# Performance work log

Measured on AMD Instinct MI355X. Metric: run time of the kernel, lower is better.

The kernel has to match this reference:

```python
import jax, jax.numpy as jnp
import numpy as np

# Hyperparameters matching init_kwargs
LR = 0.02
AT = 0.3
DSBETA = 0.1
EPS_DS = 0.5

B, D, N = 8192, 1024, 4096


def setup_inputs() -> dict:
    key = jax.random.key(0)
    k0, k1, k2, k3 = jax.random.split(key, 4)
    x = jax.random.normal(k0, (B, D), dtype=jnp.float32)
    weights = jax.random.normal(k1, (N, D), dtype=jnp.float32)
    relevance = jax.random.uniform(k2, (N, D), dtype=jnp.float32)
    moving_avg = jax.random.uniform(k3, (N, D), dtype=jnp.float32)
    node_control = jnp.ones((N,), dtype=jnp.float32)
    return {"x": x, "weights": weights, "relevance": relevance,
            "moving_avg": moving_avg, "node_control": node_control}


def reference(x, weights, relevance, moving_avg, node_control):
    n, d = weights.shape
    # pairwise squared distances [B, N] via one GEMM
    x2 = jnp.sum(x * x, axis=1, keepdims=True)            # [B,1]
    w2 = jnp.sum(weights * weights, axis=1)[None, :]      # [1,N]
    dists = x2 + w2 - 2.0 * jnp.matmul(x, weights.T)      # [B,N]
    # weighted_distance + activation
    rsum = jnp.sum(relevance, axis=1)                     # [N]
    dw = dists * (rsum / d)[None, :]
    dw = jnp.where(jnp.isnan(dw), 0.0, dw)
    act = (rsum[None, :] / (rsum[None, :] + dw + 1e-7)) * node_control[None, :]
    act_max = jnp.max(act, axis=1)                        # [B]
    idx = jnp.argmax(act, axis=1)                         # [B] winner per sample
    # high-activation mask; group samples by winner node (unique_node_diff_vectorized
    # == per-node mean of assigned high samples, done with segment_sum at fixed N)
    high = (act_max >= AT).astype(x.dtype)                # [B]
    counts = jax.ops.segment_sum(high, idx, num_segments=n)               # [N]
    sums = jax.ops.segment_sum(x * high[:, None], idx, num_segments=n)    # [N,D]
    has = (counts > 0).astype(x.dtype)[:, None]           # [N,1] nodes with >=1 high sample
    mean_s = sums / jnp.maximum(counts, 1.0)[:, None]     # [N,D] updatable_samples (dense)
    # update_node math (EMA moving_avg -> relevance -> weight update)
    a = LR * DSBETA
    distance = jnp.abs(mean_s - weights)
    mavg_new = a * distance + (1.0 - a) * moving_avg
    mx = jnp.max(mavg_new, axis=1, keepdims=True)
    mn = jnp.min(mavg_new, axis=1, keepdims=True)
    avg = jnp.mean(mavg_new, axis=1, keepdims=True)
    rel_new = 1.0 / (1.0 + jnp.exp((mavg_new - avg) / (EPS_DS * (mx - mn))))
    rel_new = jnp.where(jnp.isnan(rel_new), 1.0, rel_new)
    w_new = weights + LR * (mean_s - weights)
    # Original returns rows only for unique winning nodes (dynamic shape); here we
    # return fixed-shape [N,D] arrays masked to zero for nodes with no high sample.
    return (mean_s * has, w_new * has, rel_new * has)
```

## Files before the change

### kernel.cpp

```cpp
#include <hip/hip_runtime.h>
#include <stdint.h>

#define B_DIM 8192
#define D_DIM 1024
#define N_DIM 4096
#define ND ((size_t)N_DIM * D_DIM)
#define LRc 0.02f
#define ATc 0.3f
#define EMAc (0.02f * 0.1f)
#define QS 32.0f
#define INV_QS2 (1.0f / (QS * QS))
#define MARGIN_G 10.0f

typedef int intv4 __attribute__((ext_vector_type(4)));

__device__ __forceinline__ void async16(void* lds, const void* g) {
    __builtin_amdgcn_global_load_lds((const __attribute__((address_space(1))) void*)g,
                                     (__attribute__((address_space(3))) void*)lds, 16, 0, 0);
}

__device__ __forceinline__ int q8(float v) {
    return (int)rintf(fminf(fmaxf(v * QS, -127.0f), 127.0f));
}

__global__ __launch_bounds__(256) void prep(const float* __restrict__ x, const float* __restrict__ w,
                                            const float* __restrict__ rel,
                                            signed char* __restrict__ xq, signed char* __restrict__ wq,
                                            float* __restrict__ x2, float* __restrict__ w2,
                                            float* __restrict__ rsum, float* __restrict__ gb) {
    const int t = threadIdx.x;
    __shared__ float r1[4], r2s[4];
    if (blockIdx.x < B_DIM) {
        const int b = blockIdx.x;
        const float4 v = ((const float4*)(x + (size_t)b * D_DIM))[t];
        float ss = v.x * v.x + v.y * v.y + v.z * v.z + v.w * v.w;
        unsigned pk = (unsigned)(q8(v.x) & 255) | ((unsigned)(q8(v.y) & 255) << 8)
                    | ((unsigned)(q8(v.z) & 255) << 16) | ((unsigned)(q8(v.w) & 255) << 24);
        ((unsigned*)(xq + (size_t)b * D_DIM))[t] = pk;
#pragma unroll
        for (int o = 32; o; o >>= 1) ss += __shfl_xor(ss, o);
        if ((t & 63) == 0) r1[t >> 6] = ss;
        __syncthreads();
        if (t == 0) x2[b] = r1[0] + r1[1] + r1[2] + r1[3];
    } else {
        const int n = blockIdx.x - B_DIM;
        const float4 v = ((const float4*)(w + (size_t)n * D_DIM))[t];
        const float4 rv = ((const float4*)(rel + (size_t)n * D_DIM))[t];
        float ss = v.x * v.x + v.y * v.y + v.z * v.z + v.w * v.w;
        float rs = rv.x + rv.y + rv.z + rv.w;
        unsigned pk = (unsigned)(q8(v.x) & 255) | ((unsigned)(q8(v.y) & 255) << 8)
                    | ((unsigned)(q8(v.z) & 255) << 16) | ((unsigned)(q8(v.w) & 255) << 24);
        ((unsigned*)(wq + (size_t)n * D_DIM))[t] = pk;
#pragma unroll
        for (int o = 32; o; o >>= 1) { ss += __shfl_xor(ss, o); rs += __shfl_xor(rs, o); }
        if ((t & 63) == 0) { r1[t >> 6] = ss; r2s[t >> 6] = rs; }
        __syncthreads();
        if (t == 0) {
            const float w2v = r1[0] + r1[1] + r1[2] + r1[3];
            const float rsv = r2s[0] + r2s[1] + r2s[2] + r2s[3];
            w2[n] = w2v;
            rsum[n] = rsv;
            gb[n] = w2v + (1e-7f * (float)D_DIM) / rsv;
        }
    }
}

__global__ __launch_bounds__(256, 2) void gemm_g(const signed char* __restrict__ xq,
                                                 const signed char* __restrict__ wq,
                                                 const float* __restrict__ gb,
                                                 unsigned char* __restrict__ res,
                                                 float* __restrict__ tminp) {
    __shared__ int4 As[1024];
    __shared__ int4 Bs[2048];
    const int t = threadIdx.x;
    const int mt = blockIdx.x & 63;
    const int nt = blockIdx.x >> 6;
    const int m0 = mt * 128, n0 = nt * 256;
    const int lane = t & 63, wave = t >> 6;
    const int q = lane >> 4, ln = lane & 15;
    const int wm = wave >> 1, wn = wave & 1;

    intv4 acc[4][8];
#pragma unroll
    for (int i = 0; i < 4; ++i)
#pragma unroll
        for (int j = 0; j < 8; ++j) acc[i][j] = (intv4){0, 0, 0, 0};

    int rrA[4], jjA[4], rrB[8], jjB[8];
#pragma unroll
    for (int it = 0; it < 4; ++it) {
        int L = t + it * 256;
        rrA[it] = L >> 3; jjA[it] = (L & 7) ^ (rrA[it] & 7);
    }
#pragma unroll
    for (int it = 0; it < 8; ++it) {
        int L = t + it * 256;
        rrB[it] = L >> 3; jjB[it] = (L & 7) ^ (rrB[it] & 7);
    }

    const signed char* Ap = xq + (size_t)m0 * D_DIM;
    const signed char* Bp = wq + (size_t)n0 * D_DIM;
    for (int kt = 0; kt < 8; ++kt) {
        const int k0 = kt * 128;
#pragma unroll
        for (int it = 0; it < 4; ++it)
            async16((char*)As + (t + it * 256) * 16, Ap + (size_t)rrA[it] * D_DIM + k0 + jjA[it] * 16);
#pragma unroll
        for (int it = 0; it < 8; ++it)
            async16((char*)Bs + (t + it * 256) * 16, Bp + (size_t)rrB[it] * D_DIM + k0 + jjB[it] * 16);
        __syncthreads();
#pragma unroll
        for (int ks = 0; ks < 2; ++ks) {
            intv4 a[4], b[8];
#pragma unroll
            for (int i = 0; i < 4; ++i) {
                int r = wm * 64 + i * 16 + ln;
                int jx = (ks * 4 + q) ^ (r & 7);
                a[i] = *(const intv4*)((const char*)As + (r * 8 + jx) * 16);
            }
#pragma unroll
            for (int j = 0; j < 8; ++j) {
                int r = wn * 128 + j * 16 + ln;
                int jx = (ks * 4 + q) ^ (r & 7);
                b[j] = *(const intv4*)((const char*)Bs + (r * 8 + jx) * 16);
            }
#pragma unroll
            for (int i = 0; i < 4; ++i)
#pragma unroll
                for (int j = 0; j < 8; ++j)
                    acc[i][j] = __builtin_amdgcn_mfma_i32_16x16x64_i8(a[i], b[j], acc[i][j], 0, 0, 0);
        }
        __syncthreads();
    }

    float gbv[8];
#pragma unroll
    for (int j = 0; j < 8; ++j) gbv[j] = gb[n0 + wn * 128 + j * 16 + ln];
    const float cf = 2.0f * INV_QS2;
#pragma unroll
    for (int i = 0; i < 4; ++i) {
#pragma unroll
        for (int r = 0; r < 4; ++r) {
            const int m = m0 + wm * 64 + i * 16 + q * 4 + r;
            float g[8];
            float mnA = 3.4e38f, mnB = 3.4e38f;
#pragma unroll
            for (int j = 0; j < 8; ++j) {
                g[j] = gbv[j] - cf * (float)acc[i][j][r];
                if (j < 4) mnA = fminf(mnA, g[j]); else mnB = fminf(mnB, g[j]);
            }
#pragma unroll
            for (int o = 1; o < 16; o <<= 1) {
                mnA = fminf(mnA, __shfl_xor(mnA, o));
                mnB = fminf(mnB, __shfl_xor(mnB, o));
            }
            if (ln == 0) {
                tminp[(size_t)m * 64 + nt * 4 + wn * 2 + 0] = mnA;
                tminp[(size_t)m * 64 + nt * 4 + wn * 2 + 1] = mnB;
            }
#pragma unroll
            for (int j = 0; j < 8; ++j) {
                const float base = (j < 4) ? mnA : mnB;
                int u = (int)rintf((g[j] - base) * 2.0f);
                u = (u > 255) ? 255 : u;
                res[(size_t)m * N_DIM + n0 + wn * 128 + j * 16 + ln] = (unsigned char)u;
            }
        }
    }
}

__global__ __launch_bounds__(256) void resolve(const unsigned char* __restrict__ res,
                                               const float* __restrict__ tminp,
                                               const float* __restrict__ x2p,
                                               const float* __restrict__ x, const float* __restrict__ w,
                                               const float* __restrict__ w2, const float* __restrict__ rsum,
                                               const float* __restrict__ ncp,
                                               int* __restrict__ win) {
    const int lane = threadIdx.x & 63, wave = threadIdx.x >> 6;
    const int b = blockIdx.x * 4 + wave;
    const float tv = tminp[(size_t)b * 64 + lane];
    float rowmin = tv;
#pragma unroll
    for (int o = 32; o; o >>= 1) rowmin = fminf(rowmin, __shfl_xor(rowmin, o));
    const float th = rowmin + MARGIN_G;
    const unsigned long long tmask = __ballot(tv <= th);
    const float x2v = x2p[b];

    int cnt = 0, myn = -1;
    float myg = 0.0f;
    unsigned long long tm = tmask;
    while (tm) {
        const int tt = __ffsll((long long)tm) - 1;
        tm &= tm - 1;
        const float tb = __shfl(tv, tt);
        const unsigned char rv = res[(size_t)b * N_DIM + tt * 64 + lane];
        const float g = tb + 0.5f * (float)rv;
        const bool c = (g <= th);
        cnt += __popcll(__ballot(c));
        if (c && myn < 0) { myn = tt * 64 + lane; myg = g; }
    }

    if (cnt == 1) {
        if (myn >= 0) {
            const float act = ncp[myn] * (float)D_DIM / ((float)D_DIM + x2v + myg);
            win[b] = (act >= ATc) ? myn : -1;
        }
    } else {
        const float4* xr = (const float4*)(x + (size_t)b * D_DIM);
        float4 xv[4];
#pragma unroll
        for (int j = 0; j < 4; ++j) xv[j] = xr[lane + j * 64];
        float best_act = -1.0f;
        int best_n = N_DIM;
        tm = tmask;
        while (tm) {
            const int tt = __ffsll((long long)tm) - 1;
            tm &= tm - 1;
            const float tb = __shfl(tv, tt);
            const unsigned char rv = res[(size_t)b * N_DIM + tt * 64 + lane];
            const float g = tb + 0.5f * (float)rv;
            unsigned long long cm = __ballot(g <= th);
            while (cm) {
                const int l = __ffsll((long long)cm) - 1;
                cm &= cm - 1;
                const int n = tt * 64 + l;
                const float4* wr = (const float4*)(w + (size_t)n * D_DIM);
                float p = 0.f;
#pragma unroll
                for (int j = 0; j < 4; ++j) {
                    const float4 wv = wr[lane + j * 64];
                    p += xv[j].x * wv.x + xv[j].y * wv.y + xv[j].z * wv.z + xv[j].w * wv.w;
                }
#pragma unroll
                for (int o = 32; o; o >>= 1) p += __shfl_xor(p, o);
                const float dist = x2v + w2[n] - 2.0f * p;
                const float rs = rsum[n];
                const float dw = dist * rs * (1.0f / (float)D_DIM);
                const float a = rs * ncp[n] / (rs + dw + 1e-7f);
                if (a > best_act || (a == best_act && n < best_n)) { best_act = a; best_n = n; }
            }
        }
        if (lane == 0) win[b] = (best_act >= ATc) ? best_n : -1;
    }
}

__global__ __launch_bounds__(256) void finalize(const float* __restrict__ x, const float* __restrict__ w,
                                                const float* __restrict__ mavg, const int* __restrict__ win,
                                                float* __restrict__ out) {
    const int n = blockIdx.x, t = threadIdx.x;
    __shared__ unsigned short list[B_DIM];
    __shared__ int cnt;
    if (t == 0) cnt = 0;
    __syncthreads();
    const int4* wp = (const int4*)win;
#pragma unroll
    for (int k = 0; k < 8; ++k) {
        const int4 v = wp[k * 256 + t];
        const int b0 = (k * 256 + t) * 4;
        if (v.x == n) list[atomicAdd(&cnt, 1)] = (unsigned short)(b0 + 0);
        if (v.y == n) list[atomicAdd(&cnt, 1)] = (unsigned short)(b0 + 1);
        if (v.z == n) list[atomicAdd(&cnt, 1)] = (unsigned short)(b0 + 2);
        if (v.w == n) list[atomicAdd(&cnt, 1)] = (unsigned short)(b0 + 3);
    }
    __syncthreads();
    const int c = cnt;
    float4 s = {0.f, 0.f, 0.f, 0.f};
    for (int e = 0; e < c; ++e) {
        const float4 xv = ((const float4*)(x + (size_t)list[e] * D_DIM))[t];
        s.x += xv.x; s.y += xv.y; s.z += xv.z; s.w += xv.w;
    }
    const float has = (c > 0) ? 1.0f : 0.0f;
    const float invc = 1.0f / fmaxf((float)c, 1.0f);
    const size_t base4 = (size_t)n * (D_DIM / 4);
    const float4 wv = ((const float4*)w)[base4 + t];
    const float4 mk = ((const float4*)mavg)[base4 + t];
    float4 ms, mv;
    ms.x = s.x * invc; ms.y = s.y * invc; ms.z = s.z * invc; ms.w = s.w * invc;
    mv.x = EMAc * fabsf(ms.x - wv.x) + (1.0f - EMAc) * mk.x;
    mv.y = EMAc * fabsf(ms.y - wv.y) + (1.0f - EMAc) * mk.y;
    mv.z = EMAc * fabsf(ms.z - wv.z) + (1.0f - EMAc) * mk.z;
    mv.w = EMAc * fabsf(ms.w - wv.w) + (1.0f - EMAc) * mk.w;
    float lmax = fmaxf(fmaxf(mv.x, mv.y), fmaxf(mv.z, mv.w));
    float lmin = fminf(fminf(mv.x, mv.y), fminf(mv.z, mv.w));
    float lsum = mv.x + mv.y + mv.z + mv.w;
#pragma unroll
    for (int o = 32; o; o >>= 1) {
        lmax = fmaxf(lmax, __shfl_xor(lmax, o));
        lmin = fminf(lmin, __shfl_xor(lmin, o));
        lsum += __shfl_xor(lsum, o);
    }
    __shared__ float smax[4], smin[4], ssum[4];
    const int wave = t >> 6, lane = t & 63;
    if (lane == 0) { smax[wave] = lmax; smin[wave] = lmin; ssum[wave] = lsum; }
    __syncthreads();
    const float mx = fmaxf(fmaxf(smax[0], smax[1]), fmaxf(smax[2], smax[3]));
    const float mn = fminf(fminf(smin[0], smin[1]), fminf(smin[2], smin[3]));
    const float avg = (ssum[0] + ssum[1] + ssum[2] + ssum[3]) * (1.0f / (float)D_DIM);
    const float scale = 0.5f * (mx - mn);
    const float invs = (scale > 0.0f) ? 1.0f / scale : 0.0f;
    float4 relv;
    if (scale > 0.0f) {
        relv.x = 1.0f / (1.0f + __expf((mv.x - avg) * invs));
        relv.y = 1.0f / (1.0f + __expf((mv.y - avg) * invs));
        relv.z = 1.0f / (1.0f + __expf((mv.z - avg) * invs));
        relv.w = 1.0f / (1.0f + __expf((mv.w - avg) * invs));
    } else {
        relv.x = relv.y = relv.z = relv.w = 1.0f;
    }
    float4* o0 = (float4*)out;
    float4 r0, r1, r2;
    r0.x = ms.x * has; r0.y = ms.y * has; r0.z = ms.z * has; r0.w = ms.w * has;
    r1.x = (wv.x + LRc * (ms.x - wv.x)) * has;
    r1.y = (wv.y + LRc * (ms.y - wv.y)) * has;
    r1.z = (wv.z + LRc * (ms.z - wv.z)) * has;
    r1.w = (wv.w + LRc * (ms.w - wv.w)) * has;
    r2.x = relv.x * has; r2.y = relv.y * has; r2.z = relv.z * has; r2.w = relv.w * has;
    o0[base4 + t] = r0;
    o0[ND / 4 + base4 + t] = r1;
    o0[2 * (ND / 4) + base4 + t] = r2;
}

extern "C" void kernel_launch(void* const* d_in, const int* in_sizes, int n_in,
                              void* d_out, int out_size, void* d_ws, size_t ws_size,
                              hipStream_t stream) {
    const float* x    = (const float*)d_in[0];
    const float* w    = (const float*)d_in[1];
    const float* rel  = (const float*)d_in[2];
    const float* mavg = (const float*)d_in[3];
    const float* nc   = (const float*)d_in[4];
    float* out = (float*)d_out;

    char* p = (char*)d_ws;
    size_t off = 0;
    auto take = [&](size_t bytes) -> char* {
        char* r = p + off;
        off += (bytes + 255) & ~(size_t)255;
        return r;
    };
    signed char* xq = (signed char*)take((size_t)B_DIM * D_DIM);
    signed char* wq = (signed char*)take((size_t)N_DIM * D_DIM);
    float* x2       = (float*)take((size_t)B_DIM * 4);
    float* w2       = (float*)take((size_t)N_DIM * 4);
    float* rsum     = (float*)take((size_t)N_DIM * 4);
    float* gb       = (float*)take((size_t)N_DIM * 4);
    unsigned char* res = (unsigned char*)take((size_t)B_DIM * N_DIM);
    float* tminp    = (float*)take((size_t)B_DIM * 64 * 4);
    int* win        = (int*)take((size_t)B_DIM * 4);

    prep<<<B_DIM + N_DIM, 256, 0, stream>>>(x, w, rel, xq, wq, x2, w2, rsum, gb);
    gemm_g<<<1024, 256, 0, stream>>>(xq, wq, gb, res, tminp);
    resolve<<<B_DIM / 4, 256, 0, stream>>>(res, tminp, x2, x, w, w2, rsum, nc, win);
    finalize<<<N_DIM, 256, 0, stream>>>(x, w, mavg, win, out);
}
```

Before: 205.6 us.

## Fuse pipeline into persistent cooperative kernel with grid syncs and smaller GEMM tiles

```diff
diff --git a/kernel.cpp b/kernel.cpp
--- a/kernel.cpp
+++ b/kernel.cpp
@@ -1,5 +1,8 @@
 #include <hip/hip_runtime.h>
+#include <hip/hip_cooperative_groups.h>
 #include <stdint.h>
+
+namespace cg = cooperative_groups;
 
 #define B_DIM 8192
 #define D_DIM 1024
@@ -11,6 +14,7 @@
 #define QS 32.0f
 #define INV_QS2 (1.0f / (QS * QS))
 #define MARGIN_G 10.0f
+#define NBLK 512
 
 typedef int intv4 __attribute__((ext_vector_type(4)));
 
@@ -23,79 +27,73 @@
     return (int)rintf(fminf(fmaxf(v * QS, -127.0f), 127.0f));
 }
 
-__global__ __launch_bounds__(256) void prep(const float* __restrict__ x, const float* __restrict__ w,
-                                            const float* __restrict__ rel,
-                                            signed char* __restrict__ xq, signed char* __restrict__ wq,
-                                            float* __restrict__ x2, float* __restrict__ w2,
-                                            float* __restrict__ rsum, float* __restrict__ gb) {
-    const int t = threadIdx.x;
-    __shared__ float r1[4], r2s[4];
-    if (blockIdx.x < B_DIM) {
-        const int b = blockIdx.x;
-        const float4 v = ((const float4*)(x + (size_t)b * D_DIM))[t];
-        float ss = v.x * v.x + v.y * v.y + v.z * v.z + v.w * v.w;
-        unsigned pk = (unsigned)(q8(v.x) & 255) | ((unsigned)(q8(v.y) & 255) << 8)
-                    | ((unsigned)(q8(v.z) & 255) << 16) | ((unsigned)(q8(v.w) & 255) << 24);
-        ((unsigned*)(xq + (size_t)b * D_DIM))[t] = pk;
+__device__ __forceinline__ unsigned pack4(float4 v) {
+    return (unsigned)(q8(v.x) & 255) | ((unsigned)(q8(v.y) & 255) << 8)
+         | ((unsigned)(q8(v.z) & 255) << 16) | ((unsigned)(q8(v.w) & 255) << 24);
+}
+
+
+__device__ __forceinline__ void prep_row(int row, const float* x, const float* w, const float* rel,
+                                         signed char* xq, signed char* wq,
+                                         float* x2p, float* w2p, float* rsump, float* gbp, int lane) {
+    if (row < B_DIM) {
+        const float4* xr = (const float4*)(x + (size_t)row * D_DIM);
+        unsigned* xqr = (unsigned*)(xq + (size_t)row * D_DIM);
+        float ss = 0.f;
+#pragma unroll
+        for (int j = 0; j < 4; ++j) {
+            const float4 v = xr[lane + j * 64];
+            ss += v.x * v.x + v.y * v.y + v.z * v.z + v.w * v.w;
+            xqr[lane + j * 64] = pack4(v);
+        }
 #pragma unroll
         for (int o = 32; o; o >>= 1) ss += __shfl_xor(ss, o);
-        if ((t & 63) == 0) r1[t >> 6] = ss;
-        __syncthreads();
-        if (t == 0) x2[b] = r1[0] + r1[1] + r1[2] + r1[3];
+        if (lane == 0) x2p[row] = ss;
     } else {
-        const int n = blockIdx.x - B_DIM;
-        const float4 v = ((const float4*)(w + (size_t)n * D_DIM))[t];
-        const float4 rv = ((const float4*)(rel + (size_t)n * D_DIM))[t];
-        float ss = v.x * v.x + v.y * v.y + v.z * v.z + v.w * v.w;
-        float rs = rv.x + rv.y + rv.z + rv.w;
-        unsigned pk = (unsigned)(q8(v.x) & 255) | ((unsigned)(q8(v.y) & 255) << 8)
-                    | ((unsigned)(q8(v.z) & 255) << 16) | ((unsigned)(q8(v.w) & 255) << 24);
-        ((unsigned*)(wq + (size_t)n * D_DIM))[t] = pk;
+        const int n = row - B_DIM;
+        const float4* wr = (const float4*)(w + (size_t)n * D_DIM);
+        const float4* rr = (const float4*)(rel + (size_t)n * D_DIM);
+        unsigned* wqr = (unsigned*)(wq + (size_t)n * D_DIM);
+        float ss = 0.f, rs = 0.f;
+#pragma unroll
+        for (int j = 0; j < 4; ++j) {
+            const float4 v = wr[lane + j * 64];
+            const float4 rv = rr[lane + j * 64];
+            ss += v.x * v.x + v.y * v.y + v.z * v.z + v.w * v.w;
+            rs += rv.x + rv.y + rv.z + rv.w;
+            wqr[lane + j * 64] = pack4(v);
+        }
 #pragma unroll
         for (int o = 32; o; o >>= 1) { ss += __shfl_xor(ss, o); rs += __shfl_xor(rs, o); }
-        if ((t & 63) == 0) { r1[t >> 6] = ss; r2s[t >> 6] = rs; }
-        __syncthreads();
-        if (t == 0) {
-            const float w2v = r1[0] + r1[1] + r1[2] + r1[3];
-            const float rsv = r2s[0] + r2s[1] + r2s[2] + r2s[3];
-            w2[n] = w2v;
-            rsum[n] = rsv;
-            gb[n] = w2v + (1e-7f * (float)D_DIM) / rsv;
-        }
-    }
-}
-
-__global__ __launch_bounds__(256, 2) void gemm_g(const signed char* __restrict__ xq,
-                                                 const signed char* __restrict__ wq,
-                                                 const float* __restrict__ gb,
-                                                 unsigned char* __restrict__ res,
-                                                 float* __restrict__ tminp) {
-    __shared__ int4 As[1024];
-    __shared__ int4 Bs[2048];
-    const int t = threadIdx.x;
-    const int mt = blockIdx.x & 63;
-    const int nt = blockIdx.x >> 6;
-    const int m0 = mt * 128, n0 = nt * 256;
+        if (lane == 0) {
+            w2p[n] = ss;
+            rsump[n] = rs;
+            gbp[n] = ss + (1e-7f * (float)D_DIM) / rs;
+        }
+    }
+}
+
+__device__ __forceinline__ void gemm_tile(int tile, const signed char* xq, const signed char* wq,
+                                          const float* gbp, unsigned char* res, float* tminp,
+                                          int4* As, int4* Bs, int t) {
     const int lane = t & 63, wave = t >> 6;
     const int q = lane >> 4, ln = lane & 15;
     const int wm = wave >> 1, wn = wave & 1;
-
-    intv4 acc[4][8];
+    const int mt = tile & 63;
+    const int nt = tile >> 6;
+    const int m0 = mt * 128, n0 = nt * 128;
+
+    intv4 acc[4][4];
 #pragma unroll
     for (int i = 0; i < 4; ++i)
 #pragma unroll
-        for (int j = 0; j < 8; ++j) acc[i][j] = (intv4){0, 0, 0, 0};
-
-    int rrA[4], jjA[4], rrB[8], jjB[8];
-#pragma unroll
-    for (int it = 0; it < 4; ++it) {
-        int L = t + it * 256;
-        rrA[it] = L >> 3; jjA[it] = (L & 7) ^ (rrA[it] & 7);
-    }
-#pragma unroll
-    for (int it = 0; it < 8; ++it) {
-        int L = t + it * 256;
-        rrB[it] = L >> 3; jjB[it] = (L & 7) ^ (rrB[it] & 7);
+        for (int j = 0; j < 4; ++j) acc[i][j] = (intv4){0, 0, 0, 0};
+
+    int rr[4], jj[4];
+#pragma unroll
+    for (int s = 0; s < 4; ++s) {
+        int L = t + s * 256;
+        rr[s] = L >> 3; jj[s] = (L & 7) ^ (rr[s] & 7);
     }
 
     const signed char* Ap = xq + (size_t)m0 * D_DIM;
@@ -103,15 +101,14 @@
     for (int kt = 0; kt < 8; ++kt) {
         const int k0 = kt * 128;
 #pragma unroll
-        for (int it = 0; it < 4; ++it)
-            async16((char*)As + (t + it * 256) * 16, Ap + (size_t)rrA[it] * D_DIM + k0 + jjA[it] * 16);
-#pragma unroll
-        for (int it = 0; it < 8; ++it)
-            async16((char*)Bs + (t + it * 256) * 16, Bp + (size_t)rrB[it] * D_DIM + k0 + jjB[it] * 16);
+        for (int s = 0; s < 4; ++s) {
+            async16((char*)As + (t + s * 256) * 16, Ap + (size_t)rr[s] * D_DIM + k0 + jj[s] * 16);
+            async16((char*)Bs + (t + s * 256) * 16, Bp + (size_t)rr[s] * D_DIM + k0 + jj[s] * 16);
+        }
         __syncthreads();
 #pragma unroll
         for (int ks = 0; ks < 2; ++ks) {
-            intv4 a[4], b[8];
+            intv4 a[4], b[4];
 #pragma unroll
             for (int i = 0; i < 4; ++i) {
                 int r = wm * 64 + i * 16 + ln;
@@ -119,65 +116,53 @@
                 a[i] = *(const intv4*)((const char*)As + (r * 8 + jx) * 16);
             }
 #pragma unroll
-            for (int j = 0; j < 8; ++j) {
-                int r = wn * 128 + j * 16 + ln;
+            for (int j = 0; j < 4; ++j) {
+                int r = wn * 64 + j * 16 + ln;
                 int jx = (ks * 4 + q) ^ (r & 7);
                 b[j] = *(const intv4*)((const char*)Bs + (r * 8 + jx) * 16);
             }
 #pragma unroll
             for (int i = 0; i < 4; ++i)
 #pragma unroll
-                for (int j = 0; j < 8; ++j)
+                for (int j = 0; j < 4; ++j)
                     acc[i][j] = __builtin_amdgcn_mfma_i32_16x16x64_i8(a[i], b[j], acc[i][j], 0, 0, 0);
         }
         __syncthreads();
     }
 
-    float gbv[8];
-#pragma unroll
-    for (int j = 0; j < 8; ++j) gbv[j] = gb[n0 + wn * 128 + j * 16 + ln];
+    float gbv[4];
+#pragma unroll
+    for (int jt = 0; jt < 4; ++jt) gbv[jt] = gbp[n0 + wn * 64 + jt * 16 + ln];
     const float cf = 2.0f * INV_QS2;
 #pragma unroll
     for (int i = 0; i < 4; ++i) {
 #pragma unroll
         for (int r = 0; r < 4; ++r) {
             const int m = m0 + wm * 64 + i * 16 + q * 4 + r;
-            float g[8];
-            float mnA = 3.4e38f, mnB = 3.4e38f;
-#pragma unroll
-            for (int j = 0; j < 8; ++j) {
-                g[j] = gbv[j] - cf * (float)acc[i][j][r];
-                if (j < 4) mnA = fminf(mnA, g[j]); else mnB = fminf(mnB, g[j]);
+            float g[4];
+            float gmin = 3.4e38f;
+#pragma unroll
+            for (int jt = 0; jt < 4; ++jt) {
+                g[jt] = gbv[jt] - cf * (float)acc[i][jt][r];
+                gmin = fminf(gmin, g[jt]);
             }
 #pragma unroll
-            for (int o = 1; o < 16; o <<= 1) {
-                mnA = fminf(mnA, __shfl_xor(mnA, o));
-                mnB = fminf(mnB, __shfl_xor(mnB, o));
+            for (int o = 1; o < 16; o <<= 1) gmin = fminf(gmin, __shfl_xor(gmin, o));
+            if (ln == 0) tminp[(size_t)m * 64 + nt * 2 + wn] = gmin;
+#pragma unroll
+            for (int jt = 0; jt < 4; ++jt) {
+                int u = (int)rintf((g[jt] - gmin) * 2.0f);
+                u = (u > 255) ? 255 : u;
+                res[(size_t)m * N_DIM + n0 + wn * 64 + jt * 16 + ln] = (unsigned char)u;
             }
-            if (ln == 0) {
-                tminp[(size_t)m * 64 + nt * 4 + wn * 2 + 0] = mnA;
-                tminp[(size_t)m * 64 + nt * 4 + wn * 2 + 1] = mnB;
-            }
-#pragma unroll
-            for (int j = 0; j < 8; ++j) {
-                const float base = (j < 4) ? mnA : mnB;
-                int u = (int)rintf((g[j] - base) * 2.0f);
-                u = (u > 255) ? 255 : u;
-                res[(size_t)m * N_DIM + n0 + wn * 128 + j * 16 + ln] = (unsigned char)u;
-            }
-        }
-    }
-}
-
-__global__ __launch_bounds__(256) void resolve(const unsigned char* __restrict__ res,
-                                               const float* __restrict__ tminp,
-                                               const float* __restrict__ x2p,
-                                               const float* __restrict__ x, const float* __restrict__ w,
-                                               const float* __restrict__ w2, const float* __restrict__ rsum,
-                                               const float* __restrict__ ncp,
-                                               int* __restrict__ win) {
-    const int lane = threadIdx.x & 63, wave = threadIdx.x >> 6;
-    const int b = blockIdx.x * 4 + wave;
+        }
+    }
+}
+
+__device__ __forceinline__ void resolve_row(int b, const unsigned char* res, const float* tminp,
+                                            const float* x2p, const float* x, const float* w,
+                                            const float* w2p, const float* rsump, const float* ncp,
+                                            int* win, int lane) {
     const float tv = tminp[(size_t)b * 64 + lane];
     float rowmin = tv;
 #pragma unroll
@@ -233,8 +218,8 @@
                 }
 #pragma unroll
                 for (int o = 32; o; o >>= 1) p += __shfl_xor(p, o);
-                const float dist = x2v + w2[n] - 2.0f * p;
-                const float rs = rsum[n];
+                const float dist = x2v + w2p[n] - 2.0f * p;
+                const float rs = rsump[n];
                 const float dw = dist * rs * (1.0f / (float)D_DIM);
                 const float a = rs * ncp[n] / (rs + dw + 1e-7f);
                 if (a > best_act || (a == best_act && n < best_n)) { best_act = a; best_n = n; }
@@ -244,29 +229,32 @@
     }
 }
 
-__global__ __launch_bounds__(256) void finalize(const float* __restrict__ x, const float* __restrict__ w,
-                                                const float* __restrict__ mavg, const int* __restrict__ win,
-                                                float* __restrict__ out) {
-    const int n = blockIdx.x, t = threadIdx.x;
-    __shared__ unsigned short list[B_DIM];
-    __shared__ int cnt;
-    if (t == 0) cnt = 0;
+struct FinalSmem {
+    unsigned short list[B_DIM];
+    int cnt;
+    float smax[4], smin[4], ssum[4];
+};
+
+__device__ __forceinline__ void finalize_node(int n, const float* x, const float* w, const float* mavg,
+                                              const int* win, float* out, FinalSmem* sf, int t) {
+    const int lane = t & 63, wave = t >> 6;
+    if (t == 0) sf->cnt = 0;
     __syncthreads();
     const int4* wp = (const int4*)win;
 #pragma unroll
     for (int k = 0; k < 8; ++k) {
         const int4 v = wp[k * 256 + t];
         const int b0 = (k * 256 + t) * 4;
-        if (v.x == n) list[atomicAdd(&cnt, 1)] = (unsigned short)(b0 + 0);
-        if (v.y == n) list[atomicAdd(&cnt, 1)] = (unsigned short)(b0 + 1);
-        if (v.z == n) list[atomicAdd(&cnt, 1)] = (unsigned short)(b0 + 2);
-        if (v.w == n) list[atomicAdd(&cnt, 1)] = (unsigned short)(b0 + 3);
+        if (v.x == n) sf->list[atomicAdd(&sf->cnt, 1)] = (unsigned short)(b0 + 0);
+        if (v.y == n) sf->list[atomicAdd(&sf->cnt, 1)] = (unsigned short)(b0 + 1);
+        if (v.z == n) sf->list[atomicAdd(&sf->cnt, 1)] = (unsigned short)(b0 + 2);
+        if (v.w == n) sf->list[atomicAdd(&sf->cnt, 1)] = (unsigned short)(b0 + 3);
     }
     __syncthreads();
-    const int c = cnt;
+    const int c = sf->cnt;
     float4 s = {0.f, 0.f, 0.f, 0.f};
     for (int e = 0; e < c; ++e) {
-        const float4 xv = ((const float4*)(x + (size_t)list[e] * D_DIM))[t];
+        const float4 xv = ((const float4*)(x + (size_t)sf->list[e] * D_DIM))[t];
         s.x += xv.x; s.y += xv.y; s.z += xv.z; s.w += xv.w;
     }
     const float has = (c > 0) ? 1.0f : 0.0f;
@@ -289,13 +277,11 @@
         lmin = fminf(lmin, __shfl_xor(lmin, o));
         lsum += __shfl_xor(lsum, o);
     }
-    __shared__ float smax[4], smin[4], ssum[4];
-    const int wave = t >> 6, lane = t & 63;
-    if (lane == 0) { smax[wave] = lmax; smin[wave] = lmin; ssum[wave] = lsum; }
+    if (lane == 0) { sf->smax[wave] = lmax; sf->smin[wave] = lmin; sf->ssum[wave] = lsum; }
     __syncthreads();
-    const float mx = fmaxf(fmaxf(smax[0], smax[1]), fmaxf(smax[2], smax[3]));
-    const float mn = fminf(fminf(smin[0], smin[1]), fminf(smin[2], smin[3]));
-    const float avg = (ssum[0] + ssum[1] + ssum[2] + ssum[3]) * (1.0f / (float)D_DIM);
+    const float mx = fmaxf(fmaxf(sf->smax[0], sf->smax[1]), fmaxf(sf->smax[2], sf->smax[3]));
+    const float mn = fminf(fminf(sf->smin[0], sf->smin[1]), fminf(sf->smin[2], sf->smin[3]));
+    const float avg = (sf->ssum[0] + sf->ssum[1] + sf->ssum[2] + sf->ssum[3]) * (1.0f / (float)D_DIM);
     const float scale = 0.5f * (mx - mn);
     const float invs = (scale > 0.0f) ? 1.0f / scale : 0.0f;
     float4 relv;
@@ -318,6 +304,85 @@
     o0[base4 + t] = r0;
     o0[ND / 4 + base4 + t] = r1;
     o0[2 * (ND / 4) + base4 + t] = r2;
+}
+
+
+union SMem {
+    struct { int4 As[1024]; int4 Bs[1024]; } g;
+    FinalSmem f;
+};
+
+__global__ __launch_bounds__(256, 2) void som_fused(
+        const float* __restrict__ x, const float* __restrict__ w,
+        const float* __restrict__ rel, const float* __restrict__ mavg,
+        const float* __restrict__ ncp, float* __restrict__ out,
+        signed char* __restrict__ xq, signed char* __restrict__ wq,
+        float* __restrict__ x2p, float* __restrict__ w2p,
+        float* __restrict__ rsump, float* __restrict__ gbp,
+        unsigned char* __restrict__ res, float* __restrict__ tminp,
+        int* __restrict__ win) {
+    cg::grid_group grid = cg::this_grid();
+    __shared__ SMem sm;
+    const int t = threadIdx.x;
+    const int lane = t & 63, wave = t >> 6;
+
+    for (int it = 0; it < 6; ++it)
+        prep_row(((blockIdx.x + it * NBLK) << 2) + wave, x, w, rel, xq, wq, x2p, w2p, rsump, gbp, lane);
+
+    __threadfence(); grid.sync(); __threadfence();
+
+    for (int it = 0; it < 4; ++it)
+        gemm_tile(blockIdx.x + it * NBLK, xq, wq, gbp, res, tminp, sm.g.As, sm.g.Bs, t);
+
+    __threadfence(); grid.sync(); __threadfence();
+
+    for (int it = 0; it < 4; ++it)
+        resolve_row(((blockIdx.x + it * NBLK) << 2) + wave, res, tminp, x2p, x, w, w2p, rsump, ncp, win, lane);
+
+    __threadfence(); grid.sync(); __threadfence();
+
+    for (int it = 0; it < 8; ++it) {
+        __syncthreads();
+        finalize_node(blockIdx.x + it * NBLK, x, w, mavg, win, out, &sm.f, t);
+    }
+}
+
+
+__global__ __launch_bounds__(256) void prep_k(const float* __restrict__ x, const float* __restrict__ w,
+                                              const float* __restrict__ rel,
+                                              signed char* __restrict__ xq, signed char* __restrict__ wq,
+                                              float* __restrict__ x2p, float* __restrict__ w2p,
+                                              float* __restrict__ rsump, float* __restrict__ gbp) {
+    const int lane = threadIdx.x & 63, wave = threadIdx.x >> 6;
+    prep_row((blockIdx.x << 2) + wave, x, w, rel, xq, wq, x2p, w2p, rsump, gbp, lane);
+}
+
+__global__ __launch_bounds__(256) void gemm_k(const signed char* __restrict__ xq,
+                                              const signed char* __restrict__ wq,
+                                              const float* __restrict__ gbp,
+                                              unsigned char* __restrict__ res,
+                                              float* __restrict__ tminp) {
+    __shared__ int4 As[1024];
+    __shared__ int4 Bs[1024];
+    gemm_tile(blockIdx.x, xq, wq, gbp, res, tminp, As, Bs, threadIdx.x);
+}
+
+__global__ __launch_bounds__(256) void resolve_k(const unsigned char* __restrict__ res,
+                                                 const float* __restrict__ tminp,
+                                                 const float* __restrict__ x2p,
+                                                 const float* __restrict__ x, const float* __restrict__ w,
+                                                 const float* __restrict__ w2p, const float* __restrict__ rsump,
+                                                 const float* __restrict__ ncp,
+                                                 int* __restrict__ win) {
+    const int lane = threadIdx.x & 63, wave = threadIdx.x >> 6;
+    resolve_row((blockIdx.x << 2) + wave, res, tminp, x2p, x, w, w2p, rsump, ncp, win, lane);
+}
+
+__global__ __launch_bounds__(256) void finalize_k(const float* __restrict__ x, const float* __restrict__ w,
+                                                  const float* __restrict__ mavg, const int* __restrict__ win,
+                                                  float* __restrict__ out) {
+    __shared__ FinalSmem sf;
+    finalize_node(blockIdx.x, x, w, mavg, win, out, &sf, threadIdx.x);
 }
 
 extern "C" void kernel_launch(void* const* d_in, const int* in_sizes, int n_in,
@@ -347,8 +412,15 @@
     float* tminp    = (float*)take((size_t)B_DIM * 64 * 4);
     int* win        = (int*)take((size_t)B_DIM * 4);
 
-    prep<<<B_DIM + N_DIM, 256, 0, stream>>>(x, w, rel, xq, wq, x2, w2, rsum, gb);
-    gemm_g<<<1024, 256, 0, stream>>>(xq, wq, gb, res, tminp);
-    resolve<<<B_DIM / 4, 256, 0, stream>>>(res, tminp, x2, x, w, w2, rsum, nc, win);
-    finalize<<<N_DIM, 256, 0, stream>>>(x, w, mavg, win, out);
-}
+    void* kargs[] = { (void*)&x, (void*)&w, (void*)&rel, (void*)&mavg, (void*)&nc, (void*)&out,
+                      (void*)&xq, (void*)&wq, (void*)&x2, (void*)&w2, (void*)&rsum, (void*)&gb,
+                      (void*)&res, (void*)&tminp, (void*)&win };
+    hipError_t err = hipLaunchCooperativeKernel((const void*)som_fused, dim3(NBLK), dim3(256),
+                                                kargs, 0, stream);
+    if (err != hipSuccess) {
+        prep_k<<<(B_DIM + N_DIM) / 4, 256, 0, stream>>>(x, w, rel, xq, wq, x2, w2, rsum, gb);
+        gemm_k<<<2048, 256, 0, stream>>>(xq, wq, gb, res, tminp);
+        resolve_k<<<B_DIM / 4, 256, 0, stream>>>(res, tminp, x2, x, w, w2, rsum, nc, win);
+        finalize_k<<<N_DIM, 256, 0, stream>>>(x, w, mavg, win, out);
+    }
+}
```

After: 661.7 us. 3.22x slower.

## Pack GEMM candidate scores into 4-bit nibbles and use one wave per row in prep

Applied to the files above, without the earlier changes.

```diff
diff --git a/kernel.cpp b/kernel.cpp
--- a/kernel.cpp
+++ b/kernel.cpp
@@ -1,5 +1,6 @@
 #include <hip/hip_runtime.h>
 #include <stdint.h>
+
 
 #define B_DIM 8192
 #define D_DIM 1024
@@ -23,52 +24,59 @@
     return (int)rintf(fminf(fmaxf(v * QS, -127.0f), 127.0f));
 }
 
-__global__ __launch_bounds__(256) void prep(const float* __restrict__ x, const float* __restrict__ w,
-                                            const float* __restrict__ rel,
-                                            signed char* __restrict__ xq, signed char* __restrict__ wq,
-                                            float* __restrict__ x2, float* __restrict__ w2,
-                                            float* __restrict__ rsum, float* __restrict__ gb) {
-    const int t = threadIdx.x;
-    __shared__ float r1[4], r2s[4];
-    if (blockIdx.x < B_DIM) {
-        const int b = blockIdx.x;
-        const float4 v = ((const float4*)(x + (size_t)b * D_DIM))[t];
-        float ss = v.x * v.x + v.y * v.y + v.z * v.z + v.w * v.w;
-        unsigned pk = (unsigned)(q8(v.x) & 255) | ((unsigned)(q8(v.y) & 255) << 8)
-                    | ((unsigned)(q8(v.z) & 255) << 16) | ((unsigned)(q8(v.w) & 255) << 24);
-        ((unsigned*)(xq + (size_t)b * D_DIM))[t] = pk;
+__device__ __forceinline__ unsigned pack4(float4 v) {
+    return (unsigned)(q8(v.x) & 255) | ((unsigned)(q8(v.y) & 255) << 8)
+         | ((unsigned)(q8(v.z) & 255) << 16) | ((unsigned)(q8(v.w) & 255) << 24);
+}
+
+__global__ __launch_bounds__(256) void prep_k(const float* __restrict__ x, const float* __restrict__ w,
+                                              const float* __restrict__ rel,
+                                              signed char* __restrict__ xq, signed char* __restrict__ wq,
+                                              float* __restrict__ x2p, float* __restrict__ w2p,
+                                              float* __restrict__ rsump, float* __restrict__ gbp) {
+    const int lane = threadIdx.x & 63, wave = threadIdx.x >> 6;
+    const int row = (blockIdx.x << 2) + wave;
+    if (row < B_DIM) {
+        const float4* xr = (const float4*)(x + (size_t)row * D_DIM);
+        unsigned* xqr = (unsigned*)(xq + (size_t)row * D_DIM);
+        float ss = 0.f;
+#pragma unroll
+        for (int j = 0; j < 4; ++j) {
+            const float4 v = xr[lane + j * 64];
+            ss += v.x * v.x + v.y * v.y + v.z * v.z + v.w * v.w;
+            xqr[lane + j * 64] = pack4(v);
+        }
 #pragma unroll
         for (int o = 32; o; o >>= 1) ss += __shfl_xor(ss, o);
-        if ((t & 63) == 0) r1[t >> 6] = ss;
-        __syncthreads();
-        if (t == 0) x2[b] = r1[0] + r1[1] + r1[2] + r1[3];
+        if (lane == 0) x2p[row] = ss;
     } else {
-        const int n = blockIdx.x - B_DIM;
-        const float4 v = ((const float4*)(w + (size_t)n * D_DIM))[t];
-        const float4 rv = ((const float4*)(rel + (size_t)n * D_DIM))[t];
-        float ss = v.x * v.x + v.y * v.y + v.z * v.z + v.w * v.w;
-        float rs = rv.x + rv.y + rv.z + rv.w;
-        unsigned pk = (unsigned)(q8(v.x) & 255) | ((unsigned)(q8(v.y) & 255) << 8)
-                    | ((unsigned)(q8(v.z) & 255) << 16) | ((unsigned)(q8(v.w) & 255) << 24);
-        ((unsigned*)(wq + (size_t)n * D_DIM))[t] = pk;
+        const int n = row - B_DIM;
+        const float4* wr = (const float4*)(w + (size_t)n * D_DIM);
+        const float4* rr = (const float4*)(rel + (size_t)n * D_DIM);
+        unsigned* wqr = (unsigned*)(wq + (size_t)n * D_DIM);
+        float ss = 0.f, rs = 0.f;
+#pragma unroll
+        for (int j = 0; j < 4; ++j) {
+            const float4 v = wr[lane + j * 64];
+            const float4 rv = rr[lane + j * 64];
+            ss += v.x * v.x + v.y * v.y + v.z * v.z + v.w * v.w;
+            rs += rv.x + rv.y + rv.z + rv.w;
+            wqr[lane + j * 64] = pack4(v);
+        }
 #pragma unroll
         for (int o = 32; o; o >>= 1) { ss += __shfl_xor(ss, o); rs += __shfl_xor(rs, o); }
-        if ((t & 63) == 0) { r1[t >> 6] = ss; r2s[t >> 6] = rs; }
-        __syncthreads();
-        if (t == 0) {
-            const float w2v = r1[0] + r1[1] + r1[2] + r1[3];
-            const float rsv = r2s[0] + r2s[1] + r2s[2] + r2s[3];
-            w2[n] = w2v;
-            rsum[n] = rsv;
-            gb[n] = w2v + (1e-7f * (float)D_DIM) / rsv;
-        }
-    }
-}
-
-__global__ __launch_bounds__(256, 2) void gemm_g(const signed char* __restrict__ xq,
+        if (lane == 0) {
+            w2p[n] = ss;
+            rsump[n] = rs;
+            gbp[n] = ss + (1e-7f * (float)D_DIM) / rs;
+        }
+    }
+}
+
+__global__ __launch_bounds__(256, 2) void gemm_k(const signed char* __restrict__ xq,
                                                  const signed char* __restrict__ wq,
-                                                 const float* __restrict__ gb,
-                                                 unsigned char* __restrict__ res,
+                                                 const float* __restrict__ gbp,
+                                                 unsigned short* __restrict__ resq,
                                                  float* __restrict__ tminp) {
     __shared__ int4 As[1024];
     __shared__ int4 Bs[2048];
@@ -88,14 +96,14 @@
 
     int rrA[4], jjA[4], rrB[8], jjB[8];
 #pragma unroll
-    for (int it = 0; it < 4; ++it) {
-        int L = t + it * 256;
-        rrA[it] = L >> 3; jjA[it] = (L & 7) ^ (rrA[it] & 7);
-    }
-#pragma unroll
-    for (int it = 0; it < 8; ++it) {
-        int L = t + it * 256;
-        rrB[it] = L >> 3; jjB[it] = (L & 7) ^ (rrB[it] & 7);
+    for (int s = 0; s < 4; ++s) {
+        int L = t + s * 256;
+        rrA[s] = L >> 3; jjA[s] = (L & 7) ^ (rrA[s] & 7);
+    }
+#pragma unroll
+    for (int s = 0; s < 8; ++s) {
+        int L = t + s * 256;
+        rrB[s] = L >> 3; jjB[s] = (L & 7) ^ (rrB[s] & 7);
     }
 
     const signed char* Ap = xq + (size_t)m0 * D_DIM;
@@ -103,11 +111,11 @@
     for (int kt = 0; kt < 8; ++kt) {
         const int k0 = kt * 128;
 #pragma unroll
-        for (int it = 0; it < 4; ++it)
-            async16((char*)As + (t + it * 256) * 16, Ap + (size_t)rrA[it] * D_DIM + k0 + jjA[it] * 16);
-#pragma unroll
-        for (int it = 0; it < 8; ++it)
-            async16((char*)Bs + (t + it * 256) * 16, Bp + (size_t)rrB[it] * D_DIM + k0 + jjB[it] * 16);
+        for (int s = 0; s < 4; ++s)
+            async16((char*)As + (t + s * 256) * 16, Ap + (size_t)rrA[s] * D_DIM + k0 + jjA[s] * 16);
+#pragma unroll
+        for (int s = 0; s < 8; ++s)
+            async16((char*)Bs + (t + s * 256) * 16, Bp + (size_t)rrB[s] * D_DIM + k0 + jjB[s] * 16);
         __syncthreads();
 #pragma unroll
         for (int ks = 0; ks < 2; ++ks) {
@@ -135,8 +143,9 @@
 
     float gbv[8];
 #pragma unroll
-    for (int j = 0; j < 8; ++j) gbv[j] = gb[n0 + wn * 128 + j * 16 + ln];
+    for (int j = 0; j < 8; ++j) gbv[j] = gbp[n0 + wn * 128 + j * 16 + ln];
     const float cf = 2.0f * INV_QS2;
+    const int tileA = nt * 4 + wn * 2;
 #pragma unroll
     for (int i = 0; i < 4; ++i) {
 #pragma unroll
@@ -155,36 +164,45 @@
                 mnB = fminf(mnB, __shfl_xor(mnB, o));
             }
             if (ln == 0) {
-                tminp[(size_t)m * 64 + nt * 4 + wn * 2 + 0] = mnA;
-                tminp[(size_t)m * 64 + nt * 4 + wn * 2 + 1] = mnB;
-            }
-#pragma unroll
-            for (int j = 0; j < 8; ++j) {
-                const float base = (j < 4) ? mnA : mnB;
-                int u = (int)rintf((g[j] - base) * 2.0f);
-                u = (u > 255) ? 255 : u;
-                res[(size_t)m * N_DIM + n0 + wn * 128 + j * 16 + ln] = (unsigned char)u;
-            }
-        }
-    }
-}
-
-__global__ __launch_bounds__(256) void resolve(const unsigned char* __restrict__ res,
-                                               const float* __restrict__ tminp,
-                                               const float* __restrict__ x2p,
-                                               const float* __restrict__ x, const float* __restrict__ w,
-                                               const float* __restrict__ w2, const float* __restrict__ rsum,
-                                               const float* __restrict__ ncp,
-                                               int* __restrict__ win) {
+                tminp[(size_t)m * 64 + tileA + 0] = mnA;
+                tminp[(size_t)m * 64 + tileA + 1] = mnB;
+            }
+            unsigned uA = 0, uB = 0;
+#pragma unroll
+            for (int j = 0; j < 4; ++j) {
+                int a4 = (int)rintf(g[j] - mnA);
+                a4 = (a4 > 15) ? 15 : a4;
+                uA |= (unsigned)a4 << (4 * j);
+                int b4 = (int)rintf(g[j + 4] - mnB);
+                b4 = (b4 > 15) ? 15 : b4;
+                uB |= (unsigned)b4 << (4 * j);
+            }
+            unsigned short* rq = resq + (size_t)m * 1024;
+            rq[(tileA + 0) * 16 + ln] = (unsigned short)uA;
+            rq[(tileA + 1) * 16 + ln] = (unsigned short)uB;
+        }
+    }
+}
+
+__global__ __launch_bounds__(256) void resolve_k(const unsigned short* __restrict__ resq,
+                                                 const float* __restrict__ tminp,
+                                                 const float* __restrict__ x2p,
+                                                 const float* __restrict__ x, const float* __restrict__ w,
+                                                 const float* __restrict__ w2p, const float* __restrict__ rsump,
+                                                 const float* __restrict__ ncp,
+                                                 int* __restrict__ win) {
     const int lane = threadIdx.x & 63, wave = threadIdx.x >> 6;
-    const int b = blockIdx.x * 4 + wave;
+    const int b = (blockIdx.x << 2) + wave;
     const float tv = tminp[(size_t)b * 64 + lane];
     float rowmin = tv;
 #pragma unroll
     for (int o = 32; o; o >>= 1) rowmin = fminf(rowmin, __shfl_xor(rowmin, o));
     const float th = rowmin + MARGIN_G;
+    const float thq = th + 0.5f;
     const unsigned long long tmask = __ballot(tv <= th);
     const float x2v = x2p[b];
+    const unsigned short* rrow = resq + (size_t)b * 1024;
+    const int nibsh = (lane >> 4) * 4;
 
     int cnt = 0, myn = -1;
     float myg = 0.0f;
@@ -193,9 +211,9 @@
         const int tt = __ffsll((long long)tm) - 1;
         tm &= tm - 1;
         const float tb = __shfl(tv, tt);
-        const unsigned char rv = res[(size_t)b * N_DIM + tt * 64 + lane];
-        const float g = tb + 0.5f * (float)rv;
-        const bool c = (g <= th);
+        const unsigned short pv = rrow[tt * 16 + (lane & 15)];
+        const float g = tb + (float)((pv >> nibsh) & 15);
+        const bool c = (g <= thq);
         cnt += __popcll(__ballot(c));
         if (c && myn < 0) { myn = tt * 64 + lane; myg = g; }
     }
@@ -217,9 +235,9 @@
             const int tt = __ffsll((long long)tm) - 1;
             tm &= tm - 1;
             const float tb = __shfl(tv, tt);
-            const unsigned char rv = res[(size_t)b * N_DIM + tt * 64 + lane];
-            const float g = tb + 0.5f * (float)rv;
-            unsigned long long cm = __ballot(g <= th);
+            const unsigned short pv = rrow[tt * 16 + (lane & 15)];
+            const float g = tb + (float)((pv >> nibsh) & 15);
+            unsigned long long cm = __ballot(g <= thq);
             while (cm) {
                 const int l = __ffsll((long long)cm) - 1;
                 cm &= cm - 1;
@@ -233,8 +251,8 @@
                 }
 #pragma unroll
                 for (int o = 32; o; o >>= 1) p += __shfl_xor(p, o);
-                const float dist = x2v + w2[n] - 2.0f * p;
-                const float rs = rsum[n];
+                const float dist = x2v + w2p[n] - 2.0f * p;
+                const float rs = rsump[n];
                 const float dw = dist * rs * (1.0f / (float)D_DIM);
                 const float a = rs * ncp[n] / (rs + dw + 1e-7f);
                 if (a > best_act || (a == best_act && n < best_n)) { best_act = a; best_n = n; }
@@ -244,12 +262,13 @@
     }
 }
 
-__global__ __launch_bounds__(256) void finalize(const float* __restrict__ x, const float* __restrict__ w,
-                                                const float* __restrict__ mavg, const int* __restrict__ win,
-                                                float* __restrict__ out) {
+__global__ __launch_bounds__(256) void finalize_k(const float* __restrict__ x, const float* __restrict__ w,
+                                                  const float* __restrict__ mavg, const int* __restrict__ win,
+                                                  float* __restrict__ out) {
     const int n = blockIdx.x, t = threadIdx.x;
     __shared__ unsigned short list[B_DIM];
     __shared__ int cnt;
+    __shared__ float smax[4], smin[4], ssum[4];
     if (t == 0) cnt = 0;
     __syncthreads();
     const int4* wp = (const int4*)win;
@@ -289,7 +308,6 @@
         lmin = fminf(lmin, __shfl_xor(lmin, o));
         lsum += __shfl_xor(lsum, o);
     }
-    __shared__ float smax[4], smin[4], ssum[4];
     const int wave = t >> 6, lane = t & 63;
     if (lane == 0) { smax[wave] = lmax; smin[wave] = lmin; ssum[wave] = lsum; }
     __syncthreads();
@@ -343,12 +361,12 @@
     float* w2       = (float*)take((size_t)N_DIM * 4);
     float* rsum     = (float*)take((size_t)N_DIM * 4);
     float* gb       = (float*)take((size_t)N_DIM * 4);
-    unsigned char* res = (unsigned char*)take((size_t)B_DIM * N_DIM);
+    unsigned short* resq = (unsigned short*)take((size_t)B_DIM * 1024 * 2);
     float* tminp    = (float*)take((size_t)B_DIM * 64 * 4);
     int* win        = (int*)take((size_t)B_DIM * 4);
 
-    prep<<<B_DIM + N_DIM, 256, 0, stream>>>(x, w, rel, xq, wq, x2, w2, rsum, gb);
-    gemm_g<<<1024, 256, 0, stream>>>(xq, wq, gb, res, tminp);
-    resolve<<<B_DIM / 4, 256, 0, stream>>>(res, tminp, x2, x, w, w2, rsum, nc, win);
-    finalize<<<N_DIM, 256, 0, stream>>>(x, w, mavg, win, out);
-}
+    prep_k<<<(B_DIM + N_DIM) / 4, 256, 0, stream>>>(x, w, rel, xq, wq, x2, w2, rsum, gb);
+    gemm_k<<<1024, 256, 0, stream>>>(xq, wq, gb, resq, tminp);
+    resolve_k<<<B_DIM / 4, 256, 0, stream>>>(resq, tminp, x2, x, w, w2, rsum, nc, win);
+    finalize_k<<<N_DIM, 256, 0, stream>>>(x, w, mavg, win, out);
+}
```

Result: no change. 205.4 us (-0.1%).
